# Kernel tuning notes

Measured on AMD Instinct MI355X. Metric: run time of the kernel, lower is better.

## Reference

```python
import jax, jax.numpy as jnp
import numpy as np
import math

T_STEPS = 100   # diffusion steps
HID = 12        # hidden_dim (= per-head out_channels, concat=False)
HEADS = 4
TED = 16        # time_embed_dim
NCLS = 4        # node classes
ECLS = 2        # edge classes
N = 2048        # nodes (single graph)
E = 65536       # edges (avg degree 32)


def _sin_embed(t):
    # get_sinusoidal_embedding(t/T, TED) for a scalar t -> [1, TED]
    half = TED // 2
    scale = math.log(10000.0) / (half - 1)
    dims = jnp.exp(-jnp.arange(half, dtype=jnp.float32) * scale)
    v = (t / T_STEPS) * dims
    return jnp.concatenate([jnp.sin(v), jnp.cos(v)])[None, :]


def _tconv(x, src, dst, Wq, bq, Wk, bk, Wv, bv, Ws, bs):
    # PyG TransformerConv, heads=HEADS, concat=False, eval mode (no dropout)
    n = x.shape[0]
    q = (x @ Wq + bq).reshape(n, HEADS, HID)
    k = (x @ Wk + bk).reshape(n, HEADS, HID)
    v = (x @ Wv + bv).reshape(n, HEADS, HID)
    score = (q[dst] * k[src]).sum(-1) / np.sqrt(HID)          # [E, H]
    m = jax.ops.segment_max(score, dst, num_segments=n)       # segment softmax over dst
    m = jnp.where(jnp.isfinite(m), m, 0.0)                    # nodes with no in-edges
    e = jnp.exp(score - m[dst])
    s = jax.ops.segment_sum(e, dst, num_segments=n)
    alpha = e / (s[dst] + 1e-16)                              # PyG softmax eps
    agg = jax.ops.segment_sum(alpha[:, :, None] * v[src], dst, num_segments=n)  # [n,H,HID]
    return agg.mean(axis=1) + x @ Ws + bs                     # head-mean + root skip


def setup_inputs():
    key = jax.random.key(0)
    ks = jax.random.split(key, 32)
    def lin(i, fi, fo):
        b = 1.0 / np.sqrt(fi)
        return (jax.random.uniform(ks[i], (fi, fo), jnp.float32, -b, b),
                jax.random.uniform(ks[i + 1], (fo,), jnp.float32, -b, b))
    d_in = NCLS + TED
    H = HEADS * HID
    inp = {}
    inp["x"] = jax.nn.one_hot(jax.random.randint(ks[0], (N,), 0, NCLS), NCLS, dtype=jnp.float32)
    inp["edge_index"] = jax.random.randint(ks[1], (2, E), 0, N)
    inp["batch"] = jnp.zeros((N,), dtype=jnp.int32)
    inp["t"] = 50
    inp["time_W"], inp["time_b"] = lin(2, TED, TED)
    inp["Wq1"], inp["bq1"] = lin(4, d_in, H)
    inp["Wk1"], inp["bk1"] = lin(6, d_in, H)
    inp["Wv1"], inp["bv1"] = lin(8, d_in, H)
    inp["Ws1"], inp["bs1"] = lin(10, d_in, HID)
    inp["Wq2"], inp["bq2"] = lin(12, HID, H)
    inp["Wk2"], inp["bk2"] = lin(14, HID, H)
    inp["Wv2"], inp["bv2"] = lin(16, HID, H)
    inp["Ws2"], inp["bs2"] = lin(18, HID, HID)
    inp["Wn"], inp["bn"] = lin(20, HID, NCLS)
    inp["We1"], inp["be1"] = lin(22, 2 * HID, HID)
    inp["We2"], inp["be2"] = lin(24, HID, ECLS)
    return inp


def reference(x, edge_index, batch, t, time_W, time_b, Wq1, bq1, Wk1, bk1, Wv1, bv1, Ws1, bs1, Wq2, bq2, Wk2, bk2, Wv2, bv2, Ws2, bs2, Wn, bn, We1, be1, We2, be2):
    src, dst = edge_index[0], edge_index[1]
    te = _sin_embed(float(t)) @ time_W + time_b               # [1, TED]
    xin = jnp.concatenate([x, jnp.broadcast_to(te, (x.shape[0], TED))], axis=1)
    h = jax.nn.relu(_tconv(xin, src, dst, Wq1, bq1, Wk1, bk1, Wv1, bv1, Ws1, bs1))
    h = jax.nn.relu(_tconv(h, src, dst, Wq2, bq2, Wk2, bk2, Wv2, bv2, Ws2, bs2))
    node_logits = h @ Wn + bn
    # single graph (batch all zeros): to_dense_batch is identity, one loop iter
    n = h.shape[0]
    pairs = jnp.concatenate([jnp.broadcast_to(h[:, None, :], (n, n, HID)),
                             jnp.broadcast_to(h[None, :, :], (n, n, HID))], axis=-1)
    edge_logits = jax.nn.relu(pairs @ We1 + be1) @ We2 + be2  # [n, n, ECLS]
    return node_logits, edge_logits
```

## Files before the change

### kernel.cpp

```cpp
#include <hip/hip_runtime.h>

#define NN 2048
#define EE 65536
#define HIDD 12
#define NH 4
#define TEDD 16
#define NCLSS 4
#define H48 48
#define SLOT 128

__device__ __forceinline__ float read_t(const int* p){
  int i = *p;
  if (i >= 0 && i < 100000) return (float)i;
  return __int_as_float(i);
}

__device__ __forceinline__ void l1h(int cd, float nf0, float nf1, float nf2, float nf3,
    const float* SL, const float* vL, const float* skL, float r[HIDD])
{
  #pragma unroll
  for (int d=0; d<HIDD; d++) r[d] = 0.f;
  #pragma unroll
  for (int h=0; h<NH; h++){
    float s0 = SL[cd*16 + h*4 + 0];
    float s1 = SL[cd*16 + h*4 + 1];
    float s2 = SL[cd*16 + h*4 + 2];
    float s3 = SL[cd*16 + h*4 + 3];
    float m = -INFINITY;
    if (nf0 > 0.f) m = fmaxf(m, s0);
    if (nf1 > 0.f) m = fmaxf(m, s1);
    if (nf2 > 0.f) m = fmaxf(m, s2);
    if (nf3 > 0.f) m = fmaxf(m, s3);
    float w0 = (nf0 > 0.f) ? nf0*__expf(s0 - m) : 0.f;
    float w1 = (nf1 > 0.f) ? nf1*__expf(s1 - m) : 0.f;
    float w2 = (nf2 > 0.f) ? nf2*__expf(s2 - m) : 0.f;
    float w3 = (nf3 > 0.f) ? nf3*__expf(s3 - m) : 0.f;
    float inv = 1.0f / (w0 + w1 + w2 + w3 + 1e-16f);
    #pragma unroll
    for (int d=0; d<HIDD; d++){
      float num = w0*vL[0*H48 + h*HIDD + d] + w1*vL[1*H48 + h*HIDD + d]
                + w2*vL[2*H48 + h*HIDD + d] + w3*vL[3*H48 + h*HIDD + d];
      r[d] = fmaf(num, inv, r[d]);
    }
  }
  #pragma unroll
  for (int d=0; d<HIDD; d++)
    r[d] = fmaxf(fmaf(r[d], 0.25f, skL[cd*HIDD + d]), 0.f);
}

__global__ __launch_bounds__(512) void k_init(
    const float* __restrict__ x, const int* __restrict__ t,
    const float* __restrict__ tW, const float* __restrict__ tb,
    const float* __restrict__ Wq, const float* __restrict__ bq,
    const float* __restrict__ Wk, const float* __restrict__ bk,
    const float* __restrict__ Wv, const float* __restrict__ bv,
    const float* __restrict__ Ws, const float* __restrict__ bs,
    float* __restrict__ v1t, float* __restrict__ sk1t, float* __restrict__ Stab,
    int* __restrict__ cls, int* __restrict__ zr)
{
  const int tid = threadIdx.x;
  if (blockIdx.x > 0){
    int g = (blockIdx.x - 1)*512 + tid;
    #pragma unroll
    for (int i=g; i<NN*(1+NCLSS); i+=2048) zr[i] = 0;
    const float* xr = x + g*NCLSS;
    int c = (xr[1]>0.5f) ? 1 : ((xr[2]>0.5f) ? 2 : ((xr[3]>0.5f) ? 3 : 0));
    cls[g] = c;
    return;
  }

  __shared__ float teL[TEDD];
  __shared__ float q1tL[NCLSS][H48];
  __shared__ float k1tL[NCLSS][H48];
  if (tid < TEDD){
    float tf = read_t(t) / 100.0f;
    float lsc = __logf(10000.0f) / 7.0f;
    float emb[TEDD];
    #pragma unroll
    for (int i=0;i<8;i++){
      float vv = tf * __expf(-(float)i * lsc);
      emb[i] = __sinf(vv); emb[i+8] = __cosf(vv);
    }
    float acc = tb[tid];
    #pragma unroll
    for (int kk=0;kk<TEDD;kk++) acc = fmaf(emb[kk], tW[kk*TEDD+tid], acc);
    teL[tid] = acc;
  }
  __syncthreads();

  if (tid < NCLSS*H48){
    int c = tid / H48, j = tid - c*H48;
    float aq = bq[j] + Wq[c*H48+j];
    float ak = bk[j] + Wk[c*H48+j];
    float av = bv[j] + Wv[c*H48+j];
    #pragma unroll
    for (int d=0; d<TEDD; d++){
      float te = teL[d];
      aq = fmaf(te, Wq[(NCLSS+d)*H48+j], aq);
      ak = fmaf(te, Wk[(NCLSS+d)*H48+j], ak);
      av = fmaf(te, Wv[(NCLSS+d)*H48+j], av);
    }
    q1tL[c][j] = aq; k1tL[c][j] = ak; v1t[c*H48+j] = av;
  } else if (tid < NCLSS*H48 + NCLSS*HIDD){
    int u = tid - NCLSS*H48;
    int c = u / HIDD, j = u - c*HIDD;
    float as = bs[j] + Ws[c*HIDD+j];
    #pragma unroll
    for (int d=0; d<TEDD; d++) as = fmaf(teL[d], Ws[(NCLSS+d)*HIDD+j], as);
    sk1t[c*HIDD+j] = as;
  }
  __syncthreads();

  if (tid < 64){
    int cd = tid >> 4, h = (tid >> 2) & 3, c = tid & 3;
    float s = 0.f;
    #pragma unroll
    for (int d=0; d<HIDD; d++) s = fmaf(q1tL[cd][h*HIDD+d], k1tL[c][h*HIDD+d], s);
    Stab[tid] = s * 0.28867513459481287f;
  }
}

__global__ __launch_bounds__(512) void k_fill(
    const int* __restrict__ ei, const int* __restrict__ cls,
    int* __restrict__ cnt, int* __restrict__ ncnt, int* __restrict__ slot)
{
  int e = blockIdx.x*512 + threadIdx.x;
  int s = ei[e], d = ei[EE + e];
  int pos = atomicAdd(&cnt[d], 1);
  if (pos < SLOT) slot[d*SLOT + pos] = s;
  atomicAdd(&ncnt[d*NCLSS + cls[s]], 1);
}

__global__ __launch_bounds__(512) void k_attn(
    const int* __restrict__ cls, const int* __restrict__ cnt,
    const int* __restrict__ ncnt, const int* __restrict__ slot,
    const float* __restrict__ v1t, const float* __restrict__ sk1t,
    const float* __restrict__ Stab,
    const float* __restrict__ Wq2, const float* __restrict__ bq2,
    const float* __restrict__ Wk2, const float* __restrict__ bk2,
    const float* __restrict__ Wv2, const float* __restrict__ bv2,
    const float* __restrict__ Ws2, const float* __restrict__ bs2,
    const float* __restrict__ Wn, const float* __restrict__ bn,
    const float* __restrict__ We1, const float* __restrict__ be1,
    float* __restrict__ A, float* __restrict__ B, float* __restrict__ outNL)
{
  const int tid  = threadIdx.x;
  const int wave = tid >> 6;
  const int lane = tid & 63;
  const int head = lane >> 4;
  const int sub  = lane & 15;
  const int node = blockIdx.x*8 + wave;

  __shared__ float SL[64], vL[NCLSS*H48], skL[NCLSS*HIDD];
  __shared__ float hsw[8][64][HIDD];
  __shared__ float qw[8][H48], uw[8][H48], c0w[8][NH], skw[8][HIDD], yw[8][H48];
  if (tid < 64) SL[tid] = Stab[tid];
  else if (tid < 64 + NCLSS*H48) vL[tid-64] = v1t[tid-64];
  else if (tid < 64 + NCLSS*H48 + NCLSS*HIDD) skL[tid-64-NCLSS*H48] = sk1t[tid-64-NCLSS*H48];
  __syncthreads();

  int dg = cnt[node]; dg = (dg > SLOT) ? SLOT : dg;

  float r1[HIDD];
  {
    const int4 nc = *(const int4*)(ncnt + node*NCLSS);
    l1h(cls[node], (float)nc.x, (float)nc.y, (float)nc.z, (float)nc.w,
        SL, vL, skL, r1);
  }
  if (lane < dg && lane < 64){
    int src = slot[node*SLOT + lane];
    const int4 snc = *(const int4*)(ncnt + src*NCLSS);
    float hs[HIDD];
    l1h(cls[src], (float)snc.x, (float)snc.y, (float)snc.z, (float)snc.w,
        SL, vL, skL, hs);
    #pragma unroll
    for (int d=0; d<HIDD; d++) hsw[wave][lane][d] = hs[d];
  }

  if (lane < H48){
    float aq = bq2[lane];
    #pragma unroll
    for (int d=0; d<HIDD; d++) aq = fmaf(r1[d], Wq2[d*H48+lane], aq);
    qw[wave][lane] = aq;
  } else if (lane < H48+HIDD){
    int j = lane - H48;
    float as = bs2[j];
    #pragma unroll
    for (int d=0; d<HIDD; d++) as = fmaf(r1[d], Ws2[d*HIDD+j], as);
    skw[wave][j] = as;
  }
  __syncthreads();

  if (lane < H48){
    int h = lane / HIDD, dd = lane - h*HIDD;
    float u = 0.f;
    #pragma unroll
    for (int jj=0; jj<HIDD; jj++)
      u = fmaf(Wk2[dd*H48 + h*HIDD + jj], qw[wave][h*HIDD+jj], u);
    uw[wave][lane] = u;
  } else if (lane < H48+NH){
    int h = lane - H48;
    float c0 = 0.f;
    #pragma unroll
    for (int jj=0; jj<HIDD; jj++)
      c0 = fmaf(qw[wave][h*HIDD+jj], bk2[h*HIDD+jj], c0);
    c0w[wave][h] = c0;
  }
  __syncthreads();

  const float ksc = 0.28867513459481287f;
  float uh[HIDD];
  #pragma unroll
  for (int d=0; d<HIDD; d++) uh[d] = uw[wave][head*HIDD + d];
  const float c0h = c0w[wave][head];

  float m = -INFINITY, s = 0.f;
  float acc[HIDD];
  #pragma unroll
  for (int d=0; d<HIDD; d++) acc[d] = 0.f;

  for (int i=sub; i<dg; i+=16){
    float hs[HIDD];
    if (i < 64){
      #pragma unroll
      for (int d=0; d<HIDD; d++) hs[d] = hsw[wave][i][d];
    } else {
      int src = slot[node*SLOT + i];
      const int4 snc = *(const int4*)(ncnt + src*NCLSS);
      l1h(cls[src], (float)snc.x, (float)snc.y, (float)snc.z, (float)snc.w,
          SL, vL, skL, hs);
    }

    float sc = c0h;
    #pragma unroll
    for (int dd=0; dd<HIDD; dd++) sc = fmaf(uh[dd], hs[dd], sc);
    sc *= ksc;

    if (sc > m){
      float f = __expf(m - sc);
      s *= f;
      #pragma unroll
      for (int d=0; d<HIDD; d++) acc[d] *= f;
      m = sc;
    }
    float w = __expf(sc - m);
    s += w;
    #pragma unroll
    for (int d=0; d<HIDD; d++) acc[d] = fmaf(w, hs[d], acc[d]);
  }

  float mg = m;
  #pragma unroll
  for (int st=1; st<16; st<<=1) mg = fmaxf(mg, __shfl_xor(mg, st, 64));
  {
    float f = (m > -INFINITY) ? __expf(m - mg) : 0.f;
    s *= f;
    #pragma unroll
    for (int d=0; d<HIDD; d++) acc[d] *= f;
  }
  #pragma unroll
  for (int st=1; st<16; st<<=1){
    s += __shfl_xor(s, st, 64);
    #pragma unroll
    for (int d=0; d<HIDD; d++) acc[d] += __shfl_xor(acc[d], st, 64);
  }

  if (sub < HIDD){
    int out = head*HIDD + sub;
    float inv = 1.0f / (s + 1e-16f);
    float a2 = s * bv2[out];
    #pragma unroll
    for (int dd=0; dd<HIDD; dd++) a2 = fmaf(Wv2[dd*H48 + out], acc[dd], a2);
    yw[wave][out] = a2 * inv;
  }
  __syncthreads();

  float r2[HIDD];
  #pragma unroll
  for (int d=0; d<HIDD; d++){
    float v = yw[wave][d] + yw[wave][HIDD+d] + yw[wave][2*HIDD+d] + yw[wave][3*HIDD+d];
    r2[d] = fmaxf(fmaf(v, 0.25f, skw[wave][d]), 0.f);
  }

  if (lane < NCLSS){
    float acc2 = bn[lane];
    #pragma unroll
    for (int d=0; d<HIDD; d++) acc2 = fmaf(r2[d], Wn[d*NCLSS+lane], acc2);
    outNL[node*NCLSS + lane] = acc2;
  } else if (lane < 4 + HIDD){
    int kk = lane - 4;
    float a = be1[kk];
    #pragma unroll
    for (int d=0; d<HIDD; d++) a = fmaf(r2[d], We1[d*HIDD+kk], a);
    A[node*HIDD + kk] = a;
  } else if (lane < 4 + 2*HIDD){
    int kk = lane - 4 - HIDD;
    float bb = 0.f;
    #pragma unroll
    for (int d=0; d<HIDD; d++) bb = fmaf(r2[d], We1[(HIDD+d)*HIDD+kk], bb);
    B[node*HIDD + kk] = bb;
  }
}

__global__ __launch_bounds__(256) void k_edge(
    const float* __restrict__ A, const float* __restrict__ B,
    const float* __restrict__ We2, const float* __restrict__ be2,
    float4* __restrict__ out4)
{
  int jp = blockIdx.x*32 + (threadIdx.x & 31);
  int i0 = blockIdx.y*32 + (threadIdx.x >> 5)*4;
  float w0[HIDD], w1[HIDD], B0[HIDD], B1[HIDD];
  #pragma unroll
  for (int kk=0;kk<HIDD;kk++){ w0[kk]=We2[kk*2]; w1[kk]=We2[kk*2+1]; }
  const float* Bj = B + (size_t)jp*2*HIDD;
  #pragma unroll
  for (int kk=0;kk<HIDD;kk++){ B0[kk]=Bj[kk]; B1[kk]=Bj[HIDD+kk]; }
  float b0 = be2[0], b1 = be2[1];
  #pragma unroll
  for (int ii=0; ii<4; ii++){
    int i = i0 + ii;
    const float* Ai = A + i*HIDD;
    float c00=b0, c01=b1, c10=b0, c11=b1;
    #pragma unroll
    for (int kk=0;kk<HIDD;kk++){
      float a = Ai[kk];
      float t0 = fmaxf(a + B0[kk], 0.f);
      float t1 = fmaxf(a + B1[kk], 0.f);
      c00 = fmaf(t0, w0[kk], c00);
      c01 = fmaf(t0, w1[kk], c01);
      c10 = fmaf(t1, w0[kk], c10);
      c11 = fmaf(t1, w1[kk], c11);
    }
    float4 pr; pr.x=c00; pr.y=c01; pr.z=c10; pr.w=c11;
    out4[(size_t)i*(NN/2) + jp] = pr;
  }
}

extern "C" void kernel_launch(void* const* d_in, const int* in_sizes, int n_in,
                              void* d_out, int out_size, void* d_ws, size_t ws_size,
                              hipStream_t stream)
{
  const float* x  = (const float*)d_in[0];
  const int*  ei  = (const int*)d_in[1];
  const int*  t   = (const int*)d_in[3];
  const float* tW = (const float*)d_in[4];  const float* tb = (const float*)d_in[5];
  const float *Wq1=(const float*)d_in[6],  *bq1=(const float*)d_in[7];
  const float *Wk1=(const float*)d_in[8],  *bk1=(const float*)d_in[9];
  const float *Wv1=(const float*)d_in[10], *bv1=(const float*)d_in[11];
  const float *Ws1=(const float*)d_in[12], *bs1=(const float*)d_in[13];
  const float *Wq2=(const float*)d_in[14], *bq2=(const float*)d_in[15];
  const float *Wk2=(const float*)d_in[16], *bk2=(const float*)d_in[17];
  const float *Wv2=(const float*)d_in[18], *bv2=(const float*)d_in[19];
  const float *Ws2=(const float*)d_in[20], *bs2=(const float*)d_in[21];
  const float *Wn =(const float*)d_in[22], *bn =(const float*)d_in[23];
  const float *We1=(const float*)d_in[24], *be1=(const float*)d_in[25];
  const float *We2=(const float*)d_in[26], *be2=(const float*)d_in[27];

  float* ws = (float*)d_ws;
  float* v1t  = ws;
  float* sk1t = v1t + NCLSS*H48;
  float* Stab = sk1t + NCLSS*HIDD;
  int* cls  = (int*)(Stab + 64);
  int* cnt  = cls + NN;
  int* ncnt = cnt + NN;
  int* slot = ncnt + NN*NCLSS;
  float* A  = (float*)(slot + NN*SLOT);
  float* B  = A + NN*HIDD;

  float* outNL  = (float*)d_out;
  float4* outEL = (float4*)((float*)d_out + NN*NCLSS);

  k_init<<<5, 512, 0, stream>>>(x, t, tW, tb,
                                Wq1,bq1, Wk1,bk1, Wv1,bv1, Ws1,bs1,
                                v1t, sk1t, Stab, cls, cnt);
  k_fill<<<EE/512, 512, 0, stream>>>(ei, cls, cnt, ncnt, slot);
  k_attn<<<NN/8, 512, 0, stream>>>(cls, cnt, ncnt, slot, v1t, sk1t, Stab,
                                   Wq2,bq2, Wk2,bk2, Wv2,bv2, Ws2,bs2,
                                   Wn,bn, We1,be1, A, B, outNL);
  k_edge<<<dim3(32, 64), 256, 0, stream>>>(A, B, We2, be2, outEL);
}
```

Baseline: 49.80 us.

## Merge init and fill into block-local CSR build; recompute layer-1 tables per block

Removes the separate init and fill kernels. A new prep kernel gives each block 16 destination nodes; the block scans the whole edge list and builds counts and slots with shared-memory atomics, so no global zeroing or global atomics are needed. The layer-1 projection tables (time embedding, q/k/v/skip per class, score table) are now recomputed redundantly in every attention block instead of being read from workspace. This cuts two kernel launches, but each of 128 prep blocks rereads all 65536 destination indices, and every attention block pays extra setup compute.

```diff
diff --git a/kernel.cpp b/kernel.cpp
--- a/kernel.cpp
+++ b/kernel.cpp
@@ -13,6 +13,10 @@
   int i = *p;
   if (i >= 0 && i < 100000) return (float)i;
   return __int_as_float(i);
+}
+
+__device__ __forceinline__ int classify(const float* xr){
+  return (xr[1]>0.5f) ? 1 : ((xr[2]>0.5f) ? 2 : ((xr[3]>0.5f) ? 3 : 0));
 }
 
 __device__ __forceinline__ void l1h(int cd, float nf0, float nf1, float nf2, float nf3,
@@ -48,94 +52,49 @@
     r[d] = fmaxf(fmaf(r[d], 0.25f, skL[cd*HIDD + d]), 0.f);
 }
 
-__global__ __launch_bounds__(512) void k_init(
-    const float* __restrict__ x, const int* __restrict__ t,
+__global__ __launch_bounds__(512) void k_prep(
+    const float* __restrict__ x, const int* __restrict__ ei,
+    int* __restrict__ cls, int* __restrict__ cnt,
+    int* __restrict__ ncnt, int* __restrict__ slot)
+{
+  const int tid = threadIdx.x;
+  const int lo  = blockIdx.x * 16;
+  __shared__ int lcnt[16];
+  __shared__ int lnc[16][NCLSS];
+  if (tid < 16) lcnt[tid] = 0;
+  else if (tid >= 64 && tid < 128) lnc[(tid-64)>>2][(tid-64)&3] = 0;
+  else if (tid >= 128 && tid < 144)
+    cls[lo + tid - 128] = classify(x + (lo + tid - 128)*NCLSS);
+  __syncthreads();
+
+  for (int e = tid; e < EE; e += 512){
+    int d = ei[EE + e];
+    if ((d >> 4) == (int)blockIdx.x){
+      int s = ei[e];
+      int c = classify(x + s*NCLSS);
+      int ld = d - lo;
+      int pos = atomicAdd(&lcnt[ld], 1);
+      if (pos < SLOT) slot[d*SLOT + pos] = s;
+      atomicAdd(&lnc[ld][c], 1);
+    }
+  }
+  __syncthreads();
+  if (tid < 16) cnt[lo + tid] = lcnt[tid];
+  else if (tid >= 64 && tid < 128){
+    int u = tid - 64;
+    ncnt[(lo + (u>>2))*NCLSS + (u&3)] = lnc[u>>2][u&3];
+  }
+}
+
+__global__ __launch_bounds__(512) void k_attn(
+    const int* __restrict__ t,
     const float* __restrict__ tW, const float* __restrict__ tb,
-    const float* __restrict__ Wq, const float* __restrict__ bq,
-    const float* __restrict__ Wk, const float* __restrict__ bk,
-    const float* __restrict__ Wv, const float* __restrict__ bv,
-    const float* __restrict__ Ws, const float* __restrict__ bs,
-    float* __restrict__ v1t, float* __restrict__ sk1t, float* __restrict__ Stab,
-    int* __restrict__ cls, int* __restrict__ zr)
-{
-  const int tid = threadIdx.x;
-  if (blockIdx.x > 0){
-    int g = (blockIdx.x - 1)*512 + tid;
-    #pragma unroll
-    for (int i=g; i<NN*(1+NCLSS); i+=2048) zr[i] = 0;
-    const float* xr = x + g*NCLSS;
-    int c = (xr[1]>0.5f) ? 1 : ((xr[2]>0.5f) ? 2 : ((xr[3]>0.5f) ? 3 : 0));
-    cls[g] = c;
-    return;
-  }
-
-  __shared__ float teL[TEDD];
-  __shared__ float q1tL[NCLSS][H48];
-  __shared__ float k1tL[NCLSS][H48];
-  if (tid < TEDD){
-    float tf = read_t(t) / 100.0f;
-    float lsc = __logf(10000.0f) / 7.0f;
-    float emb[TEDD];
-    #pragma unroll
-    for (int i=0;i<8;i++){
-      float vv = tf * __expf(-(float)i * lsc);
-      emb[i] = __sinf(vv); emb[i+8] = __cosf(vv);
-    }
-    float acc = tb[tid];
-    #pragma unroll
-    for (int kk=0;kk<TEDD;kk++) acc = fmaf(emb[kk], tW[kk*TEDD+tid], acc);
-    teL[tid] = acc;
-  }
-  __syncthreads();
-
-  if (tid < NCLSS*H48){
-    int c = tid / H48, j = tid - c*H48;
-    float aq = bq[j] + Wq[c*H48+j];
-    float ak = bk[j] + Wk[c*H48+j];
-    float av = bv[j] + Wv[c*H48+j];
-    #pragma unroll
-    for (int d=0; d<TEDD; d++){
-      float te = teL[d];
-      aq = fmaf(te, Wq[(NCLSS+d)*H48+j], aq);
-      ak = fmaf(te, Wk[(NCLSS+d)*H48+j], ak);
-      av = fmaf(te, Wv[(NCLSS+d)*H48+j], av);
-    }
-    q1tL[c][j] = aq; k1tL[c][j] = ak; v1t[c*H48+j] = av;
-  } else if (tid < NCLSS*H48 + NCLSS*HIDD){
-    int u = tid - NCLSS*H48;
-    int c = u / HIDD, j = u - c*HIDD;
-    float as = bs[j] + Ws[c*HIDD+j];
-    #pragma unroll
-    for (int d=0; d<TEDD; d++) as = fmaf(teL[d], Ws[(NCLSS+d)*HIDD+j], as);
-    sk1t[c*HIDD+j] = as;
-  }
-  __syncthreads();
-
-  if (tid < 64){
-    int cd = tid >> 4, h = (tid >> 2) & 3, c = tid & 3;
-    float s = 0.f;
-    #pragma unroll
-    for (int d=0; d<HIDD; d++) s = fmaf(q1tL[cd][h*HIDD+d], k1tL[c][h*HIDD+d], s);
-    Stab[tid] = s * 0.28867513459481287f;
-  }
-}
-
-__global__ __launch_bounds__(512) void k_fill(
-    const int* __restrict__ ei, const int* __restrict__ cls,
-    int* __restrict__ cnt, int* __restrict__ ncnt, int* __restrict__ slot)
-{
-  int e = blockIdx.x*512 + threadIdx.x;
-  int s = ei[e], d = ei[EE + e];
-  int pos = atomicAdd(&cnt[d], 1);
-  if (pos < SLOT) slot[d*SLOT + pos] = s;
-  atomicAdd(&ncnt[d*NCLSS + cls[s]], 1);
-}
-
-__global__ __launch_bounds__(512) void k_attn(
+    const float* __restrict__ Wq1, const float* __restrict__ bq1,
+    const float* __restrict__ Wk1, const float* __restrict__ bk1,
+    const float* __restrict__ Wv1, const float* __restrict__ bv1,
+    const float* __restrict__ Ws1, const float* __restrict__ bs1,
     const int* __restrict__ cls, const int* __restrict__ cnt,
     const int* __restrict__ ncnt, const int* __restrict__ slot,
-    const float* __restrict__ v1t, const float* __restrict__ sk1t,
-    const float* __restrict__ Stab,
     const float* __restrict__ Wq2, const float* __restrict__ bq2,
     const float* __restrict__ Wk2, const float* __restrict__ bk2,
     const float* __restrict__ Wv2, const float* __restrict__ bv2,
@@ -151,12 +110,58 @@
   const int sub  = lane & 15;
   const int node = blockIdx.x*8 + wave;
 
+  __shared__ float teL[TEDD];
+  __shared__ float q1tL[NCLSS][H48], k1tL[NCLSS][H48];
   __shared__ float SL[64], vL[NCLSS*H48], skL[NCLSS*HIDD];
   __shared__ float hsw[8][64][HIDD];
   __shared__ float qw[8][H48], uw[8][H48], c0w[8][NH], skw[8][HIDD], yw[8][H48];
-  if (tid < 64) SL[tid] = Stab[tid];
-  else if (tid < 64 + NCLSS*H48) vL[tid-64] = v1t[tid-64];
-  else if (tid < 64 + NCLSS*H48 + NCLSS*HIDD) skL[tid-64-NCLSS*H48] = sk1t[tid-64-NCLSS*H48];
+
+  if (tid < TEDD){
+    float tf = read_t(t) / 100.0f;
+    float lsc = __logf(10000.0f) / 7.0f;
+    float emb[TEDD];
+    #pragma unroll
+    for (int i=0;i<8;i++){
+      float vv = tf * __expf(-(float)i * lsc);
+      emb[i] = __sinf(vv); emb[i+8] = __cosf(vv);
+    }
+    float acc = tb[tid];
+    #pragma unroll
+    for (int kk=0;kk<TEDD;kk++) acc = fmaf(emb[kk], tW[kk*TEDD+tid], acc);
+    teL[tid] = acc;
+  }
+  __syncthreads();
+
+  if (tid < NCLSS*H48){
+    int c = tid / H48, j = tid - c*H48;
+    float aq = bq1[j] + Wq1[c*H48+j];
+    float ak = bk1[j] + Wk1[c*H48+j];
+    float av = bv1[j] + Wv1[c*H48+j];
+    #pragma unroll
+    for (int d=0; d<TEDD; d++){
+      float te = teL[d];
+      aq = fmaf(te, Wq1[(NCLSS+d)*H48+j], aq);
+      ak = fmaf(te, Wk1[(NCLSS+d)*H48+j], ak);
+      av = fmaf(te, Wv1[(NCLSS+d)*H48+j], av);
+    }
+    q1tL[c][j] = aq; k1tL[c][j] = ak; vL[c*H48+j] = av;
+  } else if (tid < NCLSS*H48 + NCLSS*HIDD){
+    int u = tid - NCLSS*H48;
+    int c = u / HIDD, j = u - c*HIDD;
+    float as = bs1[j] + Ws1[c*HIDD+j];
+    #pragma unroll
+    for (int d=0; d<TEDD; d++) as = fmaf(teL[d], Ws1[(NCLSS+d)*HIDD+j], as);
+    skL[c*HIDD+j] = as;
+  }
+  __syncthreads();
+
+  if (tid < 64){
+    int cd = tid >> 4, h = (tid >> 2) & 3, c = tid & 3;
+    float s = 0.f;
+    #pragma unroll
+    for (int d=0; d<HIDD; d++) s = fmaf(q1tL[cd][h*HIDD+d], k1tL[c][h*HIDD+d], s);
+    SL[tid] = s * 0.28867513459481287f;
+  }
   __syncthreads();
 
   int dg = cnt[node]; dg = (dg > SLOT) ? SLOT : dg;
@@ -357,10 +362,7 @@
   const float *We2=(const float*)d_in[26], *be2=(const float*)d_in[27];
 
   float* ws = (float*)d_ws;
-  float* v1t  = ws;
-  float* sk1t = v1t + NCLSS*H48;
-  float* Stab = sk1t + NCLSS*HIDD;
-  int* cls  = (int*)(Stab + 64);
+  int* cls  = (int*)ws;
   int* cnt  = cls + NN;
   int* ncnt = cnt + NN;
   int* slot = ncnt + NN*NCLSS;
@@ -370,11 +372,10 @@
   float* outNL  = (float*)d_out;
   float4* outEL = (float4*)((float*)d_out + NN*NCLSS);
 
-  k_init<<<5, 512, 0, stream>>>(x, t, tW, tb,
-                                Wq1,bq1, Wk1,bk1, Wv1,bv1, Ws1,bs1,
-                                v1t, sk1t, Stab, cls, cnt);
-  k_fill<<<EE/512, 512, 0, stream>>>(ei, cls, cnt, ncnt, slot);
-  k_attn<<<NN/8, 512, 0, stream>>>(cls, cnt, ncnt, slot, v1t, sk1t, Stab,
+  k_prep<<<NN/16, 512, 0, stream>>>(x, ei, cls, cnt, ncnt, slot);
+  k_attn<<<NN/8, 512, 0, stream>>>(t, tW, tb,
+                                   Wq1,bq1, Wk1,bk1, Wv1,bv1, Ws1,bs1,
+                                   cls, cnt, ncnt, slot,
                                    Wq2,bq2, Wk2,bk2, Wv2,bv2, Ws2,bs2,
                                    Wn,bn, We1,be1, A, B, outNL);
   k_edge<<<dim3(32, 64), 256, 0, stream>>>(A, B, We2, be2, outEL);
```

Result: slower. 90.89 us (+82.5%).
